# Kernel tuning notes

Measured on AMD Instinct MI355X. Metric: run time of the kernel, lower is better.

Reference implementation:

```python
import jax, jax.numpy as jnp
import numpy as np


def _sqdist(x1, x2):
    # squared euclidean distance matrix, [n1, n2]
    n1 = jnp.sum(x1 * x1, axis=-1)[:, None]
    n2 = jnp.sum(x2 * x2, axis=-1)[None, :]
    d2 = n1 + n2 - 2.0 * (x1 @ x2.T)
    return jnp.maximum(d2, 0.0)


def _rbf(x1, x2, raw_length_scale, raw_variance):
    ls = jax.nn.softplus(raw_length_scale)[0]
    var = jax.nn.softplus(raw_variance)[0]
    return var * jnp.exp(-0.5 * _sqdist(x1, x2) / (ls * ls))


def setup_inputs() -> dict:
    key = jax.random.key(0)
    k1, k2, k3 = jax.random.split(key, 3)
    N_TRAIN, N_TEST, D = 4096, 8192, 8
    return {
        "x_train": jax.random.uniform(k1, (N_TRAIN, D), dtype=jnp.float32),
        "y_train": jax.random.normal(k2, (N_TRAIN,), dtype=jnp.float32),
        "w_train": jnp.ones((N_TRAIN,), dtype=jnp.float32),
        "x_test": jax.random.uniform(k3, (N_TEST, D), dtype=jnp.float32),
        "raw_length_scale": jnp.array([0.6931471824645996], dtype=jnp.float32),
        "raw_variance": jnp.array([0.6931471824645996], dtype=jnp.float32),
        "raw_noise_var": jnp.array([0.1], dtype=jnp.float32),
    }


def reference(x_train, y_train, w_train, x_test,
              raw_length_scale, raw_variance, raw_noise_var):
    n = x_train.shape[0]
    noise_var = jax.nn.softplus(raw_noise_var)[0]
    eye = jnp.eye(n, dtype=x_train.dtype)

    K = _rbf(x_train, x_train, raw_length_scale, raw_variance) + (noise_var + 1e-6) * eye

    # off-diagonal entries scaled by w_i * w_j, diagonal kept as-is
    non_diag = 1.0 - eye
    weight = w_train[:, None] * w_train[None, :]
    weighted_K = K * (non_diag * weight + eye)

    K_s = _rbf(x_train, x_test, raw_length_scale, raw_variance)
    weighted_K_s = w_train[:, None] * K_s  # diag(w) @ K_s

    K_ss = _rbf(x_test, x_test, raw_length_scale, raw_variance) \
        + 1e-6 * jnp.eye(x_test.shape[0], dtype=x_test.dtype)

    L = jnp.linalg.cholesky(weighted_K)
    alpha = jax.scipy.linalg.cho_solve((L, True), y_train[:, None])  # [n, 1]
    mu = (weighted_K_s.T @ alpha)[:, 0]  # [n_test]

    v = jax.scipy.linalg.solve_triangular(L, weighted_K_s, lower=True)  # [n, n_test]
    cov = K_ss - v.T @ v
    return mu, cov
```

## Files before the change

### kernel.cpp

```cpp
#include <hip/hip_runtime.h>
#include <math.h>

#define NT 4096
#define MT 8192
#define NB 128
#define NBLK 32
#define TBM 128
#define TBN 64
#define TBK 32
#define SRPB 64

__device__ __forceinline__ float bf2f(unsigned short h) {
  return __uint_as_float(((unsigned)h) << 16);
}
__device__ __forceinline__ float softplusf(float x) { return log1pf(expf(x)); }

__device__ __forceinline__ void load8bf(const unsigned short* __restrict__ p, float* f) {
  ushort4 u0 = *(const ushort4*)p;
  ushort4 u1 = *(const ushort4*)(p + 4);
  f[0] = bf2f(u0.x); f[1] = bf2f(u0.y); f[2] = bf2f(u0.z); f[3] = bf2f(u0.w);
  f[4] = bf2f(u1.x); f[5] = bf2f(u1.y); f[6] = bf2f(u1.z); f[7] = bf2f(u1.w);
}

__device__ __forceinline__ float getsc(const void* p, int f32) {
  return f32 ? *(const float*)p : bf2f(*(const unsigned short*)p);
}
__device__ __forceinline__ float getel(const void* p, int i, int f32) {
  return f32 ? ((const float*)p)[i] : bf2f(((const unsigned short*)p)[i]);
}
__device__ __forceinline__ void load_pt(const void* xb, int idx, int f32, float* f) {
  if (f32) {
    const float4* q = (const float4*)xb;
    float4 a = q[idx * 2], b = q[idx * 2 + 1];
    f[0] = a.x; f[1] = a.y; f[2] = a.z; f[3] = a.w;
    f[4] = b.x; f[5] = b.y; f[6] = b.z; f[7] = b.w;
  } else {
    load8bf((const unsigned short*)xb + idx * 8, f);
  }
}

__global__ void detect_dtype(const unsigned short* __restrict__ xt, int* __restrict__ flag) {
  if (threadIdx.x == 0) {
    int f = 0;
    for (int i = 0; i < 32; i++) if (xt[i] >= 0x4000) f = 1;
    flag[0] = f;
  }
}

__global__ void build_K(const void* __restrict__ xt, const void* __restrict__ w,
                        const void* __restrict__ rls, const void* __restrict__ rvar,
                        const void* __restrict__ rnv, float* __restrict__ K,
                        const int* __restrict__ flag) {
  int f32 = flag[0];
  int j = blockIdx.x * 16 + threadIdx.x;
  int i = blockIdx.y * 16 + threadIdx.y;
  float ls  = softplusf(getsc(rls, f32));
  float var = softplusf(getsc(rvar, f32));
  float cc  = -0.5f / (ls * ls);
  float v;
  if (i == j) {
    v = var + softplusf(getsc(rnv, f32)) + 1e-6f;
  } else {
    float a[8], b[8];
    load_pt(xt, i, f32, a);
    load_pt(xt, j, f32, b);
    float d = 0.f;
#pragma unroll
    for (int q = 0; q < 8; q++) { float t = a[q] - b[q]; d += t * t; }
    v = var * expf(cc * d) * getel(w, i, f32) * getel(w, j, f32);
  }
  K[(size_t)i * NT + j] = v;
}

__global__ void build_Ks(const void* __restrict__ xt, const void* __restrict__ xs,
                         const void* __restrict__ w, const void* __restrict__ rls,
                         const void* __restrict__ rvar, float* __restrict__ Ks,
                         const int* __restrict__ flag) {
  int f32 = flag[0];
  int j = blockIdx.x * 16 + threadIdx.x;
  int i = blockIdx.y * 16 + threadIdx.y;
  float ls  = softplusf(getsc(rls, f32));
  float var = softplusf(getsc(rvar, f32));
  float cc  = -0.5f / (ls * ls);
  float a[8], b[8];
  load_pt(xt, i, f32, a);
  load_pt(xs, j, f32, b);
  float d = 0.f;
#pragma unroll
  for (int q = 0; q < 8; q++) { float t = a[q] - b[q]; d += t * t; }
  Ks[(size_t)i * MT + j] = getel(w, i, f32) * var * expf(cc * d);
}

__global__ void __launch_bounds__(256) potrf_invert(float* __restrict__ Kg,
                                                    float* __restrict__ Wall, int kb) {
  __shared__ float At[NB * NB];
  __shared__ float Wv[NB * NB];
  int tid = threadIdx.x;
  int r0 = kb * NB;
  for (int idx = tid; idx < NB * NB; idx += 256) {
    int k = idx >> 7, i = idx & 127;
    At[idx] = Kg[(size_t)(r0 + k) * NT + r0 + i];
    Wv[idx] = (k == i) ? 1.f : 0.f;
  }
  __syncthreads();
  for (int j = 0; j < NB; j++) {
    float inv = 1.0f / At[j * NB + j];
    int nel = (NB - 1 - j) << 7;
    for (int idx = tid; idx < nel; idx += 256) {
      int k = j + 1 + (idx >> 7);
      int i = idx & 127;
      if (i >= k) At[k * NB + i] -= At[j * NB + i] * (At[j * NB + k] * inv);
    }
    __syncthreads();
  }
  for (int t = 0; t < NB; t++) {
    float invd = 1.0f / At[t * NB + t];
    int nel = (NB - 1 - t) << 7;
    for (int idx = tid; idx < nel; idx += 256) {
      int i = t + 1 + (idx >> 7);
      int c = idx & 127;
      Wv[i * NB + c] -= (At[t * NB + i] * invd) * Wv[t * NB + c];
    }
    __syncthreads();
  }
  for (int idx = tid; idx < NB * NB; idx += 256) {
    int k = idx >> 7, i = idx & 127;
    if (i >= k) {
      float s = sqrtf(At[k * NB + k]);
      Kg[(size_t)(r0 + i) * NT + r0 + k] = (i == k) ? s : At[idx] / s;
    }
  }
  float* Wg = Wall + (size_t)kb * NB * NB;
  for (int idx = tid; idx < NB * NB; idx += 256) {
    int i = idx >> 7;
    Wg[idx] = Wv[idx] / sqrtf(At[i * NB + i]);
  }
}

__global__ void copy_panel(const float* __restrict__ Kg, float* __restrict__ S,
                           int t0, int rows, int kb) {
  int idx = blockIdx.x * 256 + threadIdx.x;
  if (idx < rows * NB) {
    int r = idx >> 7, c = idx & 127;
    S[idx] = Kg[(size_t)(t0 + r) * NT + kb * NB + c];
  }
}

template<int SUB>
__global__ void __launch_bounds__(256) gemm_nn(const float* __restrict__ A, int lda,
                                               const float* __restrict__ B, int ldb,
                                               float* __restrict__ C, int ldc, int Kdim) {
  __shared__ float As[TBK][TBM + 4];
  __shared__ float Bs[TBK][TBN + 4];
  int tid = threadIdx.x;
  int c0 = blockIdx.x * TBN;
  int r0 = blockIdx.y * TBM;
  int tx = tid & 15, ty = tid >> 4;
  float acc[8][4];
#pragma unroll
  for (int r = 0; r < 8; r++)
#pragma unroll
    for (int c = 0; c < 4; c++) acc[r][c] = 0.f;

  int am = tid & 127, ah = tid >> 7;
  int bn = tid & 15,  bk = tid >> 4;

  for (int kt = 0; kt < Kdim; kt += TBK) {
#pragma unroll
    for (int q = 0; q < 4; q++) {
      int s = ah * 4 + q;
      float4 v = *(const float4*)&A[(size_t)(r0 + am) * lda + kt + s * 4];
      As[s * 4 + 0][am] = v.x; As[s * 4 + 1][am] = v.y;
      As[s * 4 + 2][am] = v.z; As[s * 4 + 3][am] = v.w;
    }
#pragma unroll
    for (int p = 0; p < 2; p++) {
      int kk = bk + p * 16;
      *(float4*)&Bs[kk][bn * 4] = *(const float4*)&B[(size_t)(kt + kk) * ldb + c0 + bn * 4];
    }
    __syncthreads();
#pragma unroll
    for (int k = 0; k < TBK; k++) {
      float a[8], b[4];
      *(float4*)&a[0] = *(const float4*)&As[k][ty * 8];
      *(float4*)&a[4] = *(const float4*)&As[k][ty * 8 + 4];
      *(float4*)&b[0] = *(const float4*)&Bs[k][tx * 4];
#pragma unroll
      for (int r = 0; r < 8; r++)
#pragma unroll
        for (int c = 0; c < 4; c++) acc[r][c] += a[r] * b[c];
    }
    __syncthreads();
  }
#pragma unroll
  for (int r = 0; r < 8; r++) {
    float* cp = &C[(size_t)(r0 + ty * 8 + r) * ldc + c0 + tx * 4];
    if (SUB) {
      float4 o = *(const float4*)cp;
      o.x -= acc[r][0]; o.y -= acc[r][1]; o.z -= acc[r][2]; o.w -= acc[r][3];
      *(float4*)cp = o;
    } else {
      float4 o; o.x = acc[r][0]; o.y = acc[r][1]; o.z = acc[r][2]; o.w = acc[r][3];
      *(float4*)cp = o;
    }
  }
}

template<int SUB, int SYRK>
__global__ void __launch_bounds__(256) gemm_nt(const float* __restrict__ A, int lda,
                                               const float* __restrict__ B, int ldb,
                                               float* __restrict__ C, int ldc, int Kdim) {
  int c0 = blockIdx.x * TBN;
  int r0 = blockIdx.y * TBM;
  if (SYRK && c0 > r0 + TBM - 1) return;
  __shared__ float As[TBK][TBM + 4];
  __shared__ float Bs[TBK][TBN + 4];
  int tid = threadIdx.x;
  int tx = tid & 15, ty = tid >> 4;
  float acc[8][4];
#pragma unroll
  for (int r = 0; r < 8; r++)
#pragma unroll
    for (int c = 0; c < 4; c++) acc[r][c] = 0.f;

  int am = tid & 127, ah = tid >> 7;
  int bc = tid & 63,  bh = tid >> 6;

  for (int kt = 0; kt < Kdim; kt += TBK) {
#pragma unroll
    for (int q = 0; q < 4; q++) {
      int s = ah * 4 + q;
      float4 v = *(const float4*)&A[(size_t)(r0 + am) * lda + kt + s * 4];
      As[s * 4 + 0][am] = v.x; As[s * 4 + 1][am] = v.y;
      As[s * 4 + 2][am] = v.z; As[s * 4 + 3][am] = v.w;
    }
#pragma unroll
    for (int q = 0; q < 2; q++) {
      int s = bh * 2 + q;
      float4 v = *(const float4*)&B[(size_t)(c0 + bc) * ldb + kt + s * 4];
      Bs[s * 4 + 0][bc] = v.x; Bs[s * 4 + 1][bc] = v.y;
      Bs[s * 4 + 2][bc] = v.z; Bs[s * 4 + 3][bc] = v.w;
    }
    __syncthreads();
#pragma unroll
    for (int k = 0; k < TBK; k++) {
      float a[8], b[4];
      *(float4*)&a[0] = *(const float4*)&As[k][ty * 8];
      *(float4*)&a[4] = *(const float4*)&As[k][ty * 8 + 4];
      *(float4*)&b[0] = *(const float4*)&Bs[k][tx * 4];
#pragma unroll
      for (int r = 0; r < 8; r++)
#pragma unroll
        for (int c = 0; c < 4; c++) acc[r][c] += a[r] * b[c];
    }
    __syncthreads();
  }
#pragma unroll
  for (int r = 0; r < 8; r++) {
    float* cp = &C[(size_t)(r0 + ty * 8 + r) * ldc + c0 + tx * 4];
    if (SUB) {
      float4 o = *(const float4*)cp;
      o.x -= acc[r][0]; o.y -= acc[r][1]; o.z -= acc[r][2]; o.w -= acc[r][3];
      *(float4*)cp = o;
    } else {
      float4 o; o.x = acc[r][0]; o.y = acc[r][1]; o.z = acc[r][2]; o.w = acc[r][3];
      *(float4*)cp = o;
    }
  }
}

__global__ void init_r(const void* __restrict__ y, float* __restrict__ r,
                       const int* __restrict__ flag) {
  int i = blockIdx.x * 256 + threadIdx.x;
  r[i] = getel(y, i, flag[0]);
}

__global__ void __launch_bounds__(256) fwd_step(const float* __restrict__ Lg,
                                                const float* __restrict__ Wall,
                                                float* __restrict__ r,
                                                float* __restrict__ z, int kb) {
  __shared__ float ts[NB];
  __shared__ float part[256];
  int tid = threadIdx.x;
  int r0 = kb * NB;
  {
    int row = tid >> 1, half = tid & 1;
    const float* Wr = Wall + (size_t)kb * NB * NB + row * NB + half * 64;
    const float* rv = r + r0 + half * 64;
    float acc = 0.f;
#pragma unroll
    for (int c = 0; c < 64; c += 4) {
      float4 wv = *(const float4*)&Wr[c];
      float4 xv = *(const float4*)&rv[c];
      acc += wv.x * xv.x + wv.y * xv.y + wv.z * xv.z + wv.w * xv.w;
    }
    part[tid] = acc;
    __syncthreads();
    if (half == 0) ts[row] = part[tid] + part[tid + 1];
    __syncthreads();
  }
  if (blockIdx.x == 0) {
    if (tid < NB) z[r0 + tid] = ts[tid];
    return;
  }
  int base = r0 + NB + (blockIdx.x - 1) * SRPB;
  int wv_ = tid >> 6, lane = tid & 63;
  for (int rr = wv_; rr < SRPB; rr += 4) {
    int row = base + rr;
    const float* Lr = Lg + (size_t)row * NT + r0;
    float acc = Lr[lane] * ts[lane] + Lr[lane + 64] * ts[lane + 64];
#pragma unroll
    for (int off = 32; off > 0; off >>= 1) acc += __shfl_down(acc, off, 64);
    if (lane == 0) r[row] -= acc;
  }
}

__global__ void __launch_bounds__(256) bwd_step(const float* __restrict__ Lg,
                                                const float* __restrict__ Wall,
                                                float* __restrict__ z,
                                                float* __restrict__ a, int kb) {
  __shared__ float ts[NB];
  __shared__ float part[256];
  int tid = threadIdx.x;
  int r0 = kb * NB;
  {
    int col = tid & 127, half = tid >> 7;
    const float* Wb = Wall + (size_t)kb * NB * NB;
    float acc = 0.f;
#pragma unroll 4
    for (int rr = half * 64; rr < half * 64 + 64; rr++)
      acc += Wb[rr * NB + col] * z[r0 + rr];
    part[tid] = acc;
    __syncthreads();
    if (half == 0) ts[col] = part[tid] + part[tid + 128];
    __syncthreads();
  }
  if (blockIdx.x == 0) {
    if (tid < NB) a[r0 + tid] = ts[tid];
    return;
  }
  int cb = blockIdx.x - 1;
  int col = cb * NB + (tid & 127);
  int half = tid >> 7;
  float acc = 0.f;
#pragma unroll 4
  for (int jr = half * 64; jr < half * 64 + 64; jr++)
    acc += Lg[(size_t)(r0 + jr) * NT + col] * ts[jr];
  part[tid] = acc;
  __syncthreads();
  if (half == 0) z[col] -= part[tid] + part[tid + 128];
}

__global__ void zero_mu(float* __restrict__ mu) {
  mu[blockIdx.x * 256 + threadIdx.x] = 0.f;
}
__global__ void mu_gemv(const float* __restrict__ Ks, const float* __restrict__ alpha,
                        float* __restrict__ mu) {
  int j = blockIdx.x * 256 + threadIdx.x;
  int k0 = blockIdx.y * (NT / 16);
  float s0 = 0.f, s1 = 0.f;
  for (int i = k0; i < k0 + NT / 16; i += 2) {
    s0 += Ks[(size_t)i * MT + j] * alpha[i];
    s1 += Ks[(size_t)(i + 1) * MT + j] * alpha[i + 1];
  }
  atomicAdd(&mu[j], s0 + s1);
}

__global__ void __launch_bounds__(256) cov_syrk(const float* __restrict__ V,
                                                const void* __restrict__ xs,
                                                const void* __restrict__ rls,
                                                const void* __restrict__ rvar,
                                                float* __restrict__ C,
                                                const int* __restrict__ flag) {
  int c0 = blockIdx.x * TBN;
  int r0 = blockIdx.y * TBM;
  if (r0 + TBM - 1 < c0) return;
  __shared__ float As[TBK][TBM + 4];
  __shared__ float Bs[TBK][TBN + 4];
  int f32 = flag[0];
  int tid = threadIdx.x;
  int tx = tid & 15, ty = tid >> 4;
  float acc[8][4];
#pragma unroll
  for (int r = 0; r < 8; r++)
#pragma unroll
    for (int c = 0; c < 4; c++) acc[r][c] = 0.f;

  int ak = tid >> 5, am4 = (tid & 31) * 4;
  int bk = tid >> 4, bn4 = (tid & 15) * 4;

  for (int kt = 0; kt < NT; kt += TBK) {
#pragma unroll
    for (int p = 0; p < 4; p++) {
      int kk = ak + p * 8;
      *(float4*)&As[kk][am4] = *(const float4*)&V[(size_t)(kt + kk) * MT + r0 + am4];
    }
#pragma unroll
    for (int p = 0; p < 2; p++) {
      int kk = bk + p * 16;
      *(float4*)&Bs[kk][bn4] = *(const float4*)&V[(size_t)(kt + kk) * MT + c0 + bn4];
    }
    __syncthreads();
#pragma unroll
    for (int k = 0; k < TBK; k++) {
      float a[8], b[4];
      *(float4*)&a[0] = *(const float4*)&As[k][ty * 8];
      *(float4*)&a[4] = *(const float4*)&As[k][ty * 8 + 4];
      *(float4*)&b[0] = *(const float4*)&Bs[k][tx * 4];
#pragma unroll
      for (int r = 0; r < 8; r++)
#pragma unroll
        for (int c = 0; c < 4; c++) acc[r][c] += a[r] * b[c];
    }
    __syncthreads();
  }
  float ls  = softplusf(getsc(rls, f32));
  float var = softplusf(getsc(rvar, f32));
  float cc  = -0.5f / (ls * ls);
#pragma unroll
  for (int r = 0; r < 8; r++) {
    int row = r0 + ty * 8 + r;
    float xr[8];
    load_pt(xs, row, f32, xr);
    int colb = c0 + tx * 4;
#pragma unroll
    for (int c = 0; c < 4; c++) {
      int col = colb + c;
      float xc[8];
      load_pt(xs, col, f32, xc);
      float d = 0.f;
#pragma unroll
      for (int q = 0; q < 8; q++) { float tdf = xr[q] - xc[q]; d += tdf * tdf; }
      float kss = var * expf(cc * d);
      if (row == col) kss += 1e-6f;
      float ov = kss - acc[r][c];
      if (row >= col) C[(size_t)row * MT + col] = ov;
      if (row > col)  C[(size_t)col * MT + row] = ov;
    }
  }
}

extern "C" void kernel_launch(void* const* d_in, const int* in_sizes, int n_in,
                              void* d_out, int out_size, void* d_ws, size_t ws_size,
                              hipStream_t stream) {
  (void)in_sizes; (void)n_in; (void)out_size; (void)ws_size;
  const void* xt  = d_in[0];
  const void* y   = d_in[1];
  const void* w   = d_in[2];
  const void* xs  = d_in[3];
  const void* rls = d_in[4];
  const void* rva = d_in[5];
  const void* rnv = d_in[6];

  float* mu_out  = (float*)d_out;
  float* cov_out = mu_out + MT;

  float* Kf    = (float*)d_ws;
  float* Ks    = Kf + (size_t)NT * NT;
  float* Wall  = Ks + (size_t)NT * MT;
  float* S     = Wall + (size_t)NBLK * NB * NB;
  float* rbuf  = S + (size_t)(NT - NB) * NB;
  float* zbuf  = rbuf + NT;
  float* abuf  = zbuf + NT;
  int*   flag  = (int*)(abuf + NT);

  detect_dtype<<<1, 64, 0, stream>>>((const unsigned short*)xt, flag);
  build_K<<<dim3(NT / 16, NT / 16), dim3(16, 16), 0, stream>>>(xt, w, rls, rva, rnv, Kf, flag);
  build_Ks<<<dim3(MT / 16, NT / 16), dim3(16, 16), 0, stream>>>(xt, xs, w, rls, rva, Ks, flag);

  for (int kb = 0; kb < NBLK; kb++) {
    potrf_invert<<<1, 256, 0, stream>>>(Kf, Wall, kb);
    int t0 = (kb + 1) * NB;
    int rows = NT - t0;
    if (rows > 0) {
      copy_panel<<<(rows * NB) / 256, 256, 0, stream>>>(Kf, S, t0, rows, kb);
      gemm_nt<0, 0><<<dim3(NB / TBN, rows / TBM), 256, 0, stream>>>(
          S, NB, Wall + (size_t)kb * NB * NB, NB,
          Kf + (size_t)t0 * NT + kb * NB, NT, NB);
      gemm_nt<1, 1><<<dim3(rows / TBN, rows / TBM), 256, 0, stream>>>(
          Kf + (size_t)t0 * NT + kb * NB, NT,
          Kf + (size_t)t0 * NT + kb * NB, NT,
          Kf + (size_t)t0 * NT + t0, NT, NB);
    }
  }

  init_r<<<NT / 256, 256, 0, stream>>>(y, rbuf, flag);
  for (int kb = 0; kb < NBLK; kb++) {
    int nupd = (NT - (kb + 1) * NB) / SRPB;
    fwd_step<<<1 + nupd, 256, 0, stream>>>(Kf, Wall, rbuf, zbuf, kb);
  }
  for (int kb = NBLK - 1; kb >= 0; kb--) {
    bwd_step<<<1 + kb, 256, 0, stream>>>(Kf, Wall, zbuf, abuf, kb);
  }

  zero_mu<<<MT / 256, 256, 0, stream>>>(mu_out);
  mu_gemv<<<dim3(MT / 256, 16), 256, 0, stream>>>(Ks, abuf, mu_out);

  for (int kb = 0; kb < NBLK; kb++) {
    gemm_nn<0><<<dim3(MT / TBN, 1), 256, 0, stream>>>(
        Wall + (size_t)kb * NB * NB, NB,
        Ks + (size_t)kb * NB * MT, MT,
        Ks + (size_t)kb * NB * MT, MT, NB);
    int t0 = (kb + 1) * NB;
    int rows = NT - t0;
    if (rows > 0) {
      gemm_nn<1><<<dim3(MT / TBN, rows / TBM), 256, 0, stream>>>(
          Kf + (size_t)t0 * NT + kb * NB, NT,
          Ks + (size_t)kb * NB * MT, MT,
          Ks + (size_t)t0 * MT, MT, NB);
    }
  }

  cov_syrk<<<dim3(MT / TBN, MT / TBM), 256, 0, stream>>>(Ks, xs, rls, rva, cov_out, flag);
}
```

Before: 29.27 ms.

## Use split-bf16 MFMA for triangular solve and covariance SYRK with transposed V

Replaces the fp32 SIMT GEMMs for the triangular solve of K_s and the final v^T v covariance product with MFMA bf16 kernels. Each operand is split into hi/lo bf16 pairs and combined with three MFMAs to approximate fp32 accuracy. V is now stored transposed as hi/lo bf16 planes, which halves storage per element, and mu becomes a per-row dot product. This trades extra MFMA work and per-update split/merge conversions, plus some precision loss through repeated bf16 re-splitting of V, for matrix-core throughput.

```diff
diff --git a/kernel.cpp b/kernel.cpp
--- a/kernel.cpp
+++ b/kernel.cpp
@@ -10,12 +10,25 @@
 #define TBK 32
 #define SRPB 64
 
-__device__ __forceinline__ float bf2f(unsigned short h) {
+typedef unsigned short u16;
+typedef short v8s __attribute__((ext_vector_type(8)));
+typedef float v4f __attribute__((ext_vector_type(4)));
+
+__device__ __forceinline__ float bf2f(u16 h) {
   return __uint_as_float(((unsigned)h) << 16);
 }
+__device__ __forceinline__ u16 f2bf(float x) {
+  unsigned u = __float_as_uint(x);
+  u += 0x7fffu + ((u >> 16) & 1u);
+  return (u16)(u >> 16);
+}
+__device__ __forceinline__ void split1(float x, u16& h, u16& l) {
+  h = f2bf(x);
+  l = f2bf(x - bf2f(h));
+}
 __device__ __forceinline__ float softplusf(float x) { return log1pf(expf(x)); }
 
-__device__ __forceinline__ void load8bf(const unsigned short* __restrict__ p, float* f) {
+__device__ __forceinline__ void load8bf(const u16* __restrict__ p, float* f) {
   ushort4 u0 = *(const ushort4*)p;
   ushort4 u1 = *(const ushort4*)(p + 4);
   f[0] = bf2f(u0.x); f[1] = bf2f(u0.y); f[2] = bf2f(u0.z); f[3] = bf2f(u0.w);
@@ -23,10 +36,10 @@
 }
 
 __device__ __forceinline__ float getsc(const void* p, int f32) {
-  return f32 ? *(const float*)p : bf2f(*(const unsigned short*)p);
+  return f32 ? *(const float*)p : bf2f(*(const u16*)p);
 }
 __device__ __forceinline__ float getel(const void* p, int i, int f32) {
-  return f32 ? ((const float*)p)[i] : bf2f(((const unsigned short*)p)[i]);
+  return f32 ? ((const float*)p)[i] : bf2f(((const u16*)p)[i]);
 }
 __device__ __forceinline__ void load_pt(const void* xb, int idx, int f32, float* f) {
   if (f32) {
@@ -35,11 +48,11 @@
     f[0] = a.x; f[1] = a.y; f[2] = a.z; f[3] = a.w;
     f[4] = b.x; f[5] = b.y; f[6] = b.z; f[7] = b.w;
   } else {
-    load8bf((const unsigned short*)xb + idx * 8, f);
-  }
-}
-
-__global__ void detect_dtype(const unsigned short* __restrict__ xt, int* __restrict__ flag) {
+    load8bf((const u16*)xb + idx * 8, f);
+  }
+}
+
+__global__ void detect_dtype(const u16* __restrict__ xt, int* __restrict__ flag) {
   if (threadIdx.x == 0) {
     int f = 0;
     for (int i = 0; i < 32; i++) if (xt[i] >= 0x4000) f = 1;
@@ -72,13 +85,14 @@
   K[(size_t)i * NT + j] = v;
 }
 
-__global__ void build_Ks(const void* __restrict__ xt, const void* __restrict__ xs,
-                         const void* __restrict__ w, const void* __restrict__ rls,
-                         const void* __restrict__ rvar, float* __restrict__ Ks,
-                         const int* __restrict__ flag) {
+__global__ void build_Kst(const void* __restrict__ xt, const void* __restrict__ xs,
+                          const void* __restrict__ w, const void* __restrict__ rls,
+                          const void* __restrict__ rvar,
+                          u16* __restrict__ hi, u16* __restrict__ lo,
+                          const int* __restrict__ flag) {
   int f32 = flag[0];
-  int j = blockIdx.x * 16 + threadIdx.x;
-  int i = blockIdx.y * 16 + threadIdx.y;
+  int i = blockIdx.x * 16 + threadIdx.x;
+  int j = blockIdx.y * 16 + threadIdx.y;
   float ls  = softplusf(getsc(rls, f32));
   float var = softplusf(getsc(rvar, f32));
   float cc  = -0.5f / (ls * ls);
@@ -88,7 +102,10 @@
   float d = 0.f;
 #pragma unroll
   for (int q = 0; q < 8; q++) { float t = a[q] - b[q]; d += t * t; }
-  Ks[(size_t)i * MT + j] = getel(w, i, f32) * var * expf(cc * d);
+  float v = getel(w, i, f32) * var * expf(cc * d);
+  size_t o = (size_t)j * NT + i;
+  u16 h, l; split1(v, h, l);
+  hi[o] = h; lo[o] = l;
 }
 
 __global__ void __launch_bounds__(256) potrf_invert(float* __restrict__ Kg,
@@ -143,66 +160,6 @@
   if (idx < rows * NB) {
     int r = idx >> 7, c = idx & 127;
     S[idx] = Kg[(size_t)(t0 + r) * NT + kb * NB + c];
-  }
-}
-
-template<int SUB>
-__global__ void __launch_bounds__(256) gemm_nn(const float* __restrict__ A, int lda,
-                                               const float* __restrict__ B, int ldb,
-                                               float* __restrict__ C, int ldc, int Kdim) {
-  __shared__ float As[TBK][TBM + 4];
-  __shared__ float Bs[TBK][TBN + 4];
-  int tid = threadIdx.x;
-  int c0 = blockIdx.x * TBN;
-  int r0 = blockIdx.y * TBM;
-  int tx = tid & 15, ty = tid >> 4;
-  float acc[8][4];
-#pragma unroll
-  for (int r = 0; r < 8; r++)
-#pragma unroll
-    for (int c = 0; c < 4; c++) acc[r][c] = 0.f;
-
-  int am = tid & 127, ah = tid >> 7;
-  int bn = tid & 15,  bk = tid >> 4;
-
-  for (int kt = 0; kt < Kdim; kt += TBK) {
-#pragma unroll
-    for (int q = 0; q < 4; q++) {
-      int s = ah * 4 + q;
-      float4 v = *(const float4*)&A[(size_t)(r0 + am) * lda + kt + s * 4];
-      As[s * 4 + 0][am] = v.x; As[s * 4 + 1][am] = v.y;
-      As[s * 4 + 2][am] = v.z; As[s * 4 + 3][am] = v.w;
-    }
-#pragma unroll
-    for (int p = 0; p < 2; p++) {
-      int kk = bk + p * 16;
-      *(float4*)&Bs[kk][bn * 4] = *(const float4*)&B[(size_t)(kt + kk) * ldb + c0 + bn * 4];
-    }
-    __syncthreads();
-#pragma unroll
-    for (int k = 0; k < TBK; k++) {
-      float a[8], b[4];
-      *(float4*)&a[0] = *(const float4*)&As[k][ty * 8];
-      *(float4*)&a[4] = *(const float4*)&As[k][ty * 8 + 4];
-      *(float4*)&b[0] = *(const float4*)&Bs[k][tx * 4];
-#pragma unroll
-      for (int r = 0; r < 8; r++)
-#pragma unroll
-        for (int c = 0; c < 4; c++) acc[r][c] += a[r] * b[c];
-    }
-    __syncthreads();
-  }
-#pragma unroll
-  for (int r = 0; r < 8; r++) {
-    float* cp = &C[(size_t)(r0 + ty * 8 + r) * ldc + c0 + tx * 4];
-    if (SUB) {
-      float4 o = *(const float4*)cp;
-      o.x -= acc[r][0]; o.y -= acc[r][1]; o.z -= acc[r][2]; o.w -= acc[r][3];
-      *(float4*)cp = o;
-    } else {
-      float4 o; o.x = acc[r][0]; o.y = acc[r][1]; o.z = acc[r][2]; o.w = acc[r][3];
-      *(float4*)cp = o;
-    }
   }
 }
 
@@ -351,91 +308,195 @@
   if (half == 0) z[col] -= part[tid] + part[tid + 128];
 }
 
-__global__ void zero_mu(float* __restrict__ mu) {
-  mu[blockIdx.x * 256 + threadIdx.x] = 0.f;
-}
-__global__ void mu_gemv(const float* __restrict__ Ks, const float* __restrict__ alpha,
-                        float* __restrict__ mu) {
-  int j = blockIdx.x * 256 + threadIdx.x;
-  int k0 = blockIdx.y * (NT / 16);
-  float s0 = 0.f, s1 = 0.f;
-  for (int i = k0; i < k0 + NT / 16; i += 2) {
-    s0 += Ks[(size_t)i * MT + j] * alpha[i];
-    s1 += Ks[(size_t)(i + 1) * MT + j] * alpha[i + 1];
-  }
-  atomicAdd(&mu[j], s0 + s1);
-}
-
-__global__ void __launch_bounds__(256) cov_syrk(const float* __restrict__ V,
-                                                const void* __restrict__ xs,
-                                                const void* __restrict__ rls,
-                                                const void* __restrict__ rvar,
-                                                float* __restrict__ C,
-                                                const int* __restrict__ flag) {
-  int c0 = blockIdx.x * TBN;
-  int r0 = blockIdx.y * TBM;
-  if (r0 + TBM - 1 < c0) return;
-  __shared__ float As[TBK][TBM + 4];
-  __shared__ float Bs[TBK][TBN + 4];
-  int f32 = flag[0];
+__global__ void conv_W(const float* __restrict__ src, u16* __restrict__ hi,
+                       u16* __restrict__ lo) {
+  int idx = (blockIdx.x * 256 + threadIdx.x) * 4;
+  float4 v = *(const float4*)&src[idx];
+  ushort4 h, l;
+  split1(v.x, h.x, l.x); split1(v.y, h.y, l.y);
+  split1(v.z, h.z, l.z); split1(v.w, h.w, l.w);
+  *(ushort4*)&hi[idx] = h;
+  *(ushort4*)&lo[idx] = l;
+}
+
+__global__ void __launch_bounds__(256) mu_dot(const u16* __restrict__ hi,
+                                              const u16* __restrict__ lo,
+                                              const float* __restrict__ alpha,
+                                              float* __restrict__ mu) {
+  int lane = threadIdx.x & 63, wv = threadIdx.x >> 6;
+  int j = blockIdx.x * 4 + wv;
+  const u16* ph = hi + (size_t)j * NT;
+  const u16* pl = lo + (size_t)j * NT;
+  float s = 0.f;
+  for (int c = lane * 4; c < NT; c += 256) {
+    ushort4 h = *(const ushort4*)&ph[c];
+    ushort4 l = *(const ushort4*)&pl[c];
+    float4 a = *(const float4*)&alpha[c];
+    s += (bf2f(h.x) + bf2f(l.x)) * a.x + (bf2f(h.y) + bf2f(l.y)) * a.y
+       + (bf2f(h.z) + bf2f(l.z)) * a.z + (bf2f(h.w) + bf2f(l.w)) * a.w;
+  }
+#pragma unroll
+  for (int off = 32; off > 0; off >>= 1) s += __shfl_down(s, off, 64);
+  if (lane == 0) mu[j] = s;
+}
+
+template<int MODE, int BF32>
+__global__ void __launch_bounds__(256) mm_bf16(
+    const u16* __restrict__ Ah, const u16* __restrict__ Al, int lda,
+    const u16* __restrict__ Bh, const u16* __restrict__ Bl,
+    const float* __restrict__ Bf, int ldb,
+    u16* __restrict__ Chi, u16* __restrict__ Clo, float* __restrict__ Cf,
+    int ldc, int Kdim,
+    const void* __restrict__ xs, const void* __restrict__ rls,
+    const void* __restrict__ rvar, const int* __restrict__ flag) {
+  int c0 = blockIdx.x * 128;
+  int r0 = blockIdx.y * 128;
+  if (MODE == 2 && r0 < c0) return;
+  __shared__ u16 L[4][128 * 64];
   int tid = threadIdx.x;
-  int tx = tid & 15, ty = tid >> 4;
-  float acc[8][4];
-#pragma unroll
-  for (int r = 0; r < 8; r++)
-#pragma unroll
-    for (int c = 0; c < 4; c++) acc[r][c] = 0.f;
-
-  int ak = tid >> 5, am4 = (tid & 31) * 4;
-  int bk = tid >> 4, bn4 = (tid & 15) * 4;
-
-  for (int kt = 0; kt < NT; kt += TBK) {
+  int lane = tid & 63, wv = tid >> 6;
+  int wr = wv >> 1, wc = wv & 1;
+  int lr = lane & 15, lk = lane >> 4;
+
+  v4f acc[4][4];
+  v4f zero = {0.f, 0.f, 0.f, 0.f};
+#pragma unroll
+  for (int mi = 0; mi < 4; mi++)
+#pragma unroll
+    for (int ni = 0; ni < 4; ni++) acc[mi][ni] = zero;
+
+  for (int kt = 0; kt < Kdim; kt += 64) {
+    int4 rga[8], rgb[8];
 #pragma unroll
     for (int p = 0; p < 4; p++) {
-      int kk = ak + p * 8;
-      *(float4*)&As[kk][am4] = *(const float4*)&V[(size_t)(kt + kk) * MT + r0 + am4];
-    }
-#pragma unroll
-    for (int p = 0; p < 2; p++) {
-      int kk = bk + p * 16;
-      *(float4*)&Bs[kk][bn4] = *(const float4*)&V[(size_t)(kt + kk) * MT + c0 + bn4];
-    }
-    __syncthreads();
-#pragma unroll
-    for (int k = 0; k < TBK; k++) {
-      float a[8], b[4];
-      *(float4*)&a[0] = *(const float4*)&As[k][ty * 8];
-      *(float4*)&a[4] = *(const float4*)&As[k][ty * 8 + 4];
-      *(float4*)&b[0] = *(const float4*)&Bs[k][tx * 4];
-#pragma unroll
-      for (int r = 0; r < 8; r++)
-#pragma unroll
-        for (int c = 0; c < 4; c++) acc[r][c] += a[r] * b[c];
-    }
-    __syncthreads();
-  }
-  float ls  = softplusf(getsc(rls, f32));
-  float var = softplusf(getsc(rvar, f32));
-  float cc  = -0.5f / (ls * ls);
-#pragma unroll
-  for (int r = 0; r < 8; r++) {
-    int row = r0 + ty * 8 + r;
-    float xr[8];
-    load_pt(xs, row, f32, xr);
-    int colb = c0 + tx * 4;
-#pragma unroll
-    for (int c = 0; c < 4; c++) {
-      int col = colb + c;
-      float xc[8];
-      load_pt(xs, col, f32, xc);
-      float d = 0.f;
-#pragma unroll
-      for (int q = 0; q < 8; q++) { float tdf = xr[q] - xc[q]; d += tdf * tdf; }
-      float kss = var * expf(cc * d);
-      if (row == col) kss += 1e-6f;
-      float ov = kss - acc[r][c];
-      if (row >= col) C[(size_t)row * MT + col] = ov;
-      if (row > col)  C[(size_t)col * MT + row] = ov;
+      int ch = p * 256 + tid;
+      int row = ch >> 3, sl = ch & 7;
+      size_t o = (size_t)(r0 + row) * lda + kt + sl * 8;
+      rga[p]     = *(const int4*)(Ah + o);
+      rga[p + 4] = *(const int4*)(Al + o);
+    }
+    if (BF32 == 0) {
+#pragma unroll
+      for (int p = 0; p < 4; p++) {
+        int ch = p * 256 + tid;
+        int row = ch >> 3, sl = ch & 7;
+        size_t o = (size_t)(c0 + row) * ldb + kt + sl * 8;
+        rgb[p]     = *(const int4*)(Bh + o);
+        rgb[p + 4] = *(const int4*)(Bl + o);
+      }
+    } else {
+#pragma unroll
+      for (int p = 0; p < 8; p++) {
+        int ch = p * 256 + tid;
+        int row = ch >> 4, f4 = ch & 15;
+        rgb[p] = *(const int4*)(Bf + (size_t)(c0 + row) * ldb + kt + f4 * 4);
+      }
+    }
+    __syncthreads();
+#pragma unroll
+    for (int p = 0; p < 4; p++) {
+      int ch = p * 256 + tid;
+      int row = ch >> 3, sl = ch & 7;
+      int off = row * 64 + ((sl ^ (row & 7)) * 8);
+      *(int4*)&L[0][off] = rga[p];
+      *(int4*)&L[1][off] = rga[p + 4];
+      if (BF32 == 0) {
+        *(int4*)&L[2][off] = rgb[p];
+        *(int4*)&L[3][off] = rgb[p + 4];
+      }
+    }
+    if (BF32 == 1) {
+#pragma unroll
+      for (int p = 0; p < 8; p++) {
+        int ch = p * 256 + tid;
+        int row = ch >> 4, f4 = ch & 15;
+        const float* v = (const float*)&rgb[p];
+        ushort4 h, l;
+        split1(v[0], h.x, l.x); split1(v[1], h.y, l.y);
+        split1(v[2], h.z, l.z); split1(v[3], h.w, l.w);
+        int sl = f4 >> 1, half = f4 & 1;
+        int off = row * 64 + ((sl ^ (row & 7)) * 8) + half * 4;
+        *(ushort4*)&L[2][off] = h;
+        *(ushort4*)&L[3][off] = l;
+      }
+    }
+    __syncthreads();
+#pragma unroll
+    for (int ks = 0; ks < 2; ks++) {
+      v8s afh[4], afl[4], bfh[4], bfl[4];
+#pragma unroll
+      for (int mi = 0; mi < 4; mi++) {
+        int row = wr * 64 + mi * 16 + lr;
+        int sl = (ks * 4 + lk) ^ (row & 7);
+        afh[mi] = *(const v8s*)&L[0][row * 64 + sl * 8];
+        afl[mi] = *(const v8s*)&L[1][row * 64 + sl * 8];
+      }
+#pragma unroll
+      for (int ni = 0; ni < 4; ni++) {
+        int row = wc * 64 + ni * 16 + lr;
+        int sl = (ks * 4 + lk) ^ (row & 7);
+        bfh[ni] = *(const v8s*)&L[2][row * 64 + sl * 8];
+        bfl[ni] = *(const v8s*)&L[3][row * 64 + sl * 8];
+      }
+#pragma unroll
+      for (int mi = 0; mi < 4; mi++)
+#pragma unroll
+        for (int ni = 0; ni < 4; ni++) {
+          acc[mi][ni] = __builtin_amdgcn_mfma_f32_16x16x32_bf16(afh[mi], bfh[ni], acc[mi][ni], 0, 0, 0);
+          acc[mi][ni] = __builtin_amdgcn_mfma_f32_16x16x32_bf16(afh[mi], bfl[ni], acc[mi][ni], 0, 0, 0);
+          acc[mi][ni] = __builtin_amdgcn_mfma_f32_16x16x32_bf16(afl[mi], bfh[ni], acc[mi][ni], 0, 0, 0);
+        }
+    }
+  }
+
+  if (MODE == 2) {
+    int f32 = flag[0];
+    float ls  = softplusf(getsc(rls, f32));
+    float var = softplusf(getsc(rvar, f32));
+    float cc  = -0.5f / (ls * ls);
+#pragma unroll
+    for (int mi = 0; mi < 4; mi++) {
+#pragma unroll
+      for (int r = 0; r < 4; r++) {
+        int grow = r0 + wr * 64 + mi * 16 + lk * 4 + r;
+        float xr[8];
+        load_pt(xs, grow, f32, xr);
+#pragma unroll
+        for (int ni = 0; ni < 4; ni++) {
+          int gcol = c0 + wc * 64 + ni * 16 + lr;
+          float xc[8];
+          load_pt(xs, gcol, f32, xc);
+          float d = 0.f;
+#pragma unroll
+          for (int q = 0; q < 8; q++) { float t = xr[q] - xc[q]; d += t * t; }
+          float kss = var * expf(cc * d);
+          if (grow == gcol) kss += 1e-6f;
+          float ov = kss - acc[mi][ni][r];
+          Cf[(size_t)grow * ldc + gcol] = ov;
+          if (grow > gcol) Cf[(size_t)gcol * ldc + grow] = ov;
+        }
+      }
+    }
+  } else {
+#pragma unroll
+    for (int mi = 0; mi < 4; mi++) {
+#pragma unroll
+      for (int r = 0; r < 4; r++) {
+        int grow = r0 + wr * 64 + mi * 16 + lk * 4 + r;
+#pragma unroll
+        for (int ni = 0; ni < 4; ni++) {
+          int gcol = c0 + wc * 64 + ni * 16 + lr;
+          size_t o = (size_t)grow * ldc + gcol;
+          float nv;
+          if (MODE == 0) {
+            nv = acc[mi][ni][r];
+          } else {
+            nv = (bf2f(Chi[o]) + bf2f(Clo[o])) - acc[mi][ni][r];
+          }
+          u16 h, l; split1(nv, h, l);
+          Chi[o] = h; Clo[o] = l;
+        }
+      }
     }
   }
 }
@@ -455,18 +516,22 @@
   float* mu_out  = (float*)d_out;
   float* cov_out = mu_out + MT;
 
-  float* Kf    = (float*)d_ws;
-  float* Ks    = Kf + (size_t)NT * NT;
-  float* Wall  = Ks + (size_t)NT * MT;
-  float* S     = Wall + (size_t)NBLK * NB * NB;
-  float* rbuf  = S + (size_t)(NT - NB) * NB;
-  float* zbuf  = rbuf + NT;
-  float* abuf  = zbuf + NT;
-  int*   flag  = (int*)(abuf + NT);
-
-  detect_dtype<<<1, 64, 0, stream>>>((const unsigned short*)xt, flag);
+  float* Kf   = (float*)d_ws;
+  float* Wall = Kf + (size_t)NT * NT;
+  float* S    = Wall + (size_t)NBLK * NB * NB;
+  float* rbuf = S + (size_t)(NT - NB) * NB;
+  float* zbuf = rbuf + NT;
+  float* abuf = zbuf + NT;
+  int*   flag = (int*)(abuf + NT);
+  u16* Whi  = (u16*)(flag + 4);
+  u16* Wlo  = Whi + (size_t)NBLK * NB * NB;
+  u16* Vthi = Wlo + (size_t)NBLK * NB * NB;
+  u16* Vtlo = Vthi + (size_t)MT * NT;
+
+  detect_dtype<<<1, 64, 0, stream>>>((const u16*)xt, flag);
   build_K<<<dim3(NT / 16, NT / 16), dim3(16, 16), 0, stream>>>(xt, w, rls, rva, rnv, Kf, flag);
-  build_Ks<<<dim3(MT / 16, NT / 16), dim3(16, 16), 0, stream>>>(xt, xs, w, rls, rva, Ks, flag);
+  build_Kst<<<dim3(NT / 16, MT / 16), dim3(16, 16), 0, stream>>>(xt, xs, w, rls, rva,
+                                                                 Vthi, Vtlo, flag);
 
   for (int kb = 0; kb < NBLK; kb++) {
     potrf_invert<<<1, 256, 0, stream>>>(Kf, Wall, kb);
@@ -484,6 +549,8 @@
     }
   }
 
+  conv_W<<<(NBLK * NB * NB) / 1024, 256, 0, stream>>>(Wall, Whi, Wlo);
+
   init_r<<<NT / 256, 256, 0, stream>>>(y, rbuf, flag);
   for (int kb = 0; kb < NBLK; kb++) {
     int nupd = (NT - (kb + 1) * NB) / SRPB;
@@ -493,23 +560,27 @@
     bwd_step<<<1 + kb, 256, 0, stream>>>(Kf, Wall, zbuf, abuf, kb);
   }
 
-  zero_mu<<<MT / 256, 256, 0, stream>>>(mu_out);
-  mu_gemv<<<dim3(MT / 256, 16), 256, 0, stream>>>(Ks, abuf, mu_out);
+  mu_dot<<<MT / 4, 256, 0, stream>>>(Vthi, Vtlo, abuf, mu_out);
 
   for (int kb = 0; kb < NBLK; kb++) {
-    gemm_nn<0><<<dim3(MT / TBN, 1), 256, 0, stream>>>(
-        Wall + (size_t)kb * NB * NB, NB,
-        Ks + (size_t)kb * NB * MT, MT,
-        Ks + (size_t)kb * NB * MT, MT, NB);
+    mm_bf16<0, 0><<<dim3(1, MT / 128), 256, 0, stream>>>(
+        Vthi + kb * NB, Vtlo + kb * NB, NT,
+        Whi + (size_t)kb * NB * NB, Wlo + (size_t)kb * NB * NB, nullptr, NB,
+        Vthi + kb * NB, Vtlo + kb * NB, nullptr, NT, NB,
+        nullptr, nullptr, nullptr, nullptr);
     int t0 = (kb + 1) * NB;
     int rows = NT - t0;
     if (rows > 0) {
-      gemm_nn<1><<<dim3(MT / TBN, rows / TBM), 256, 0, stream>>>(
-          Kf + (size_t)t0 * NT + kb * NB, NT,
-          Ks + (size_t)kb * NB * MT, MT,
-          Ks + (size_t)t0 * MT, MT, NB);
-    }
-  }
-
-  cov_syrk<<<dim3(MT / TBN, MT / TBM), 256, 0, stream>>>(Ks, xs, rls, rva, cov_out, flag);
-}
+      mm_bf16<1, 1><<<dim3(rows / 128, MT / 128), 256, 0, stream>>>(
+          Vthi + kb * NB, Vtlo + kb * NB, NT,
+          nullptr, nullptr, Kf + (size_t)t0 * NT + kb * NB, NT,
+          Vthi + t0, Vtlo + t0, nullptr, NT, NB,
+          nullptr, nullptr, nullptr, nullptr);
+    }
+  }
+
+  mm_bf16<2, 0><<<dim3(MT / 128, MT / 128), 256, 0, stream>>>(
+      Vthi, Vtlo, NT, Vthi, Vtlo, nullptr, NT,
+      nullptr, nullptr, cov_out, MT, NT,
+      xs, rls, rva, flag);
+}
```

Measured after the change: 29.35 ms. No clear change (+0.3%).
